# Performance work log

Measured on AMD Instinct MI355X. Metric: run time of the kernel, lower is better.

## Reference

```python
import jax, jax.numpy as jnp
import numpy as np
import math

H = 8
C = 512
HIDE = 2048
LN_EPS = 1e-6


def setup_inputs() -> dict:
    key = jax.random.key(0)
    ks = jax.random.split(key, 9)
    B, N = 4, 2048
    std = 0.02
    return {
        "q": jax.random.normal(ks[0], (B, N, C), jnp.float32),
        "k": jax.random.normal(ks[1], (B, N, C), jnp.float32),
        "v": jax.random.normal(ks[2], (B, N, C), jnp.float32),
        "fc1_w": jax.random.normal(ks[3], (HIDE, C), jnp.float32) * std,
        "fc1_b": jnp.zeros((HIDE,), jnp.float32),
        "fc2_w": jax.random.normal(ks[4], (C, HIDE), jnp.float32) * std,
        "fc2_b": jnp.zeros((C,), jnp.float32),
        "ln1_w": jnp.ones((C,), jnp.float32),
        "ln1_b": jnp.zeros((C,), jnp.float32),
        "ln2_w": jnp.ones((C,), jnp.float32),
        "ln2_b": jnp.zeros((C,), jnp.float32),
    }


def _layernorm(x, w, b):
    mu = jnp.mean(x, axis=-1, keepdims=True)
    var = jnp.var(x, axis=-1, keepdims=True)
    return (x - mu) * jax.lax.rsqrt(var + LN_EPS) * w + b


def _mha(q, k, v):
    B, N, _ = q.shape
    hd = C // H
    # [B, H, N, hd]
    qh = q.reshape(B, N, H, hd).transpose(0, 2, 1, 3)
    kh = k.reshape(B, N, H, hd).transpose(0, 2, 1, 3)
    vh = v.reshape(B, N, H, hd).transpose(0, 2, 1, 3)
    scores = jnp.einsum('bhqd,bhkd->bhqk', qh, kh) / math.sqrt(hd)
    probs = jax.nn.softmax(scores, axis=-1)
    out = jnp.einsum('bhqk,bhkd->bhqd', probs, vh)
    return out.transpose(0, 2, 1, 3).reshape(B, N, C)


def reference(q, k, v, fc1_w, fc1_b, fc2_w, fc2_b, ln1_w, ln1_b, ln2_w, ln2_b):
    attn = _mha(q, k, v)
    q2 = _layernorm(q + attn, ln1_w, ln1_b)
    h = jax.nn.gelu(q2 @ fc1_w.T + fc1_b, approximate=False)
    mlp = h @ fc2_w.T + fc2_b
    return _layernorm(q2 + mlp, ln2_w, ln2_b)
```

## Files before the change

kernel.cpp:

```cpp
#include <hip/hip_runtime.h>
#include <math.h>

typedef unsigned short u16;
typedef __bf16 bf16_t;
typedef bf16_t bf16x4 __attribute__((ext_vector_type(4)));
typedef bf16_t bf16x8 __attribute__((ext_vector_type(8)));
typedef short s16x4 __attribute__((ext_vector_type(4)));
typedef float f32x4 __attribute__((ext_vector_type(4)));

typedef const __attribute__((address_space(1))) void* gcp;
typedef __attribute__((address_space(3))) void* lcp;

#define BB 4
#define NN 2048
#define CC 512
#define HH 8
#define HD 64
#define HIDE_ 2048
#define TT (BB*NN)

#if __has_builtin(__builtin_amdgcn_exp2f)
#define EXP2(x) __builtin_amdgcn_exp2f(x)
#else
#define EXP2(x) __expf((x) * 0.69314718055994531f)
#endif

#if __has_builtin(__builtin_amdgcn_rcpf)
#define RCP(x) __builtin_amdgcn_rcpf(x)
#else
#define RCP(x) (1.0f / (x))
#endif

__device__ __forceinline__ u16 f2bf(float f) {
  unsigned u = __float_as_uint(f);
  u += 0x7FFF + ((u >> 16) & 1);
  return (u16)(u >> 16);
}

__device__ __forceinline__ int xcd_swz(int orig, int nwg) {
  return (orig & 7) * (nwg >> 3) + (orig >> 3);
}

__device__ __forceinline__ void bf8_to_f(const u16* p, float* f) {
  uint4 u = *(const uint4*)p;
  f[0] = __uint_as_float(u.x << 16); f[1] = __uint_as_float(u.x & 0xffff0000u);
  f[2] = __uint_as_float(u.y << 16); f[3] = __uint_as_float(u.y & 0xffff0000u);
  f[4] = __uint_as_float(u.z << 16); f[5] = __uint_as_float(u.z & 0xffff0000u);
  f[6] = __uint_as_float(u.w << 16); f[7] = __uint_as_float(u.w & 0xffff0000u);
}

__device__ __forceinline__ bf16x8 ldq8(const float* p, float s) {
  float4 a = *(const float4*)p;
  float4 b = *(const float4*)(p + 4);
  bf16x8 r = {(bf16_t)(a.x * s), (bf16_t)(a.y * s), (bf16_t)(a.z * s), (bf16_t)(a.w * s),
              (bf16_t)(b.x * s), (bf16_t)(b.y * s), (bf16_t)(b.z * s), (bf16_t)(b.w * s)};
  return r;
}

__device__ __forceinline__ float gelu_tanh(float x) {
  float y = 0.7978845608028654f * x * (1.0f + 0.044715f * x * x);
  float a = y * 2.8853900817779268f;
  a = fminf(fmaxf(a, -30.0f), 30.0f);
  float e = EXP2(a);
  float t = (e - 1.0f) * RCP(e + 1.0f);
  return 0.5f * x * (1.0f + t);
}

__global__ __launch_bounds__(256) void prep_kernel(const float* __restrict__ k,
                                                   const float* __restrict__ fc1w,
                                                   const float* __restrict__ fc2w,
                                                   const float* __restrict__ v,
                                                   u16* __restrict__ kb,
                                                   u16* __restrict__ w1b,
                                                   u16* __restrict__ w2b,
                                                   u16* __restrict__ vtb) {
  __shared__ __align__(16) u16 T[64 * 72];
  int bid = blockIdx.x, tid = threadIdx.x;
  if (bid < 3072) {
    const float* in;
    u16* out;
    int rel;
    if (bid < 2048)      { in = k;    out = kb;  rel = bid; }
    else if (bid < 2560) { in = fc1w; out = w1b; rel = bid - 2048; }
    else                 { in = fc2w; out = w2b; rel = bid - 2560; }
    int i = (rel * 256 + tid) * 8;
    float4 a = *(const float4*)(in + i);
    float4 b2 = *(const float4*)(in + i + 4);
    u16 r[8] = {f2bf(a.x), f2bf(a.y), f2bf(a.z), f2bf(a.w),
                f2bf(b2.x), f2bf(b2.y), f2bf(b2.z), f2bf(b2.w)};
    *(uint4*)(out + i) = *(const uint4*)r;
    return;
  }
  int tv = bid - 3072;
  int j0 = (tv & 31) * 64;
  int bh = tv >> 5;
  int b = bh >> 3, h = bh & 7;
#pragma unroll
  for (int i = 0; i < 16; i++) {
    int idx = i * 256 + tid;
    int j = idx >> 6, d = idx & 63;
    T[d * 72 + j] = f2bf(v[((size_t)(b * NN + j0 + j)) * CC + h * 64 + d]);
  }
  __syncthreads();
#pragma unroll
  for (int i = 0; i < 16; i++) {
    int idx = i * 256 + tid;
    int d = idx >> 6, j = idx & 63;
    vtb[((size_t)(bh * 64 + d)) * NN + j0 + j] = T[d * 72 + j];
  }
}

__global__ __launch_bounds__(256, 4) void attn_kernel(const float* __restrict__ qf,
                                                      const u16* __restrict__ kb,
                                                      const u16* __restrict__ vtb,
                                                      u16* __restrict__ ou,
                                                      float* __restrict__ lsum,
                                                      float qs) {
  __shared__ __align__(16) u16 Ks[64 * 64];
  __shared__ __align__(16) u16 Vs[64 * 64];
  int tid = threadIdx.x, wave = tid >> 6, lane = tid & 63;
  int l15 = lane & 15, quad = lane >> 4;
  int r7 = l15 & 7;
  int bid = xcd_swz(blockIdx.x, 512);
  int half = blockIdx.y;
  int qt = bid & 15, h = (bid >> 4) & 7, b = bid >> 7;
  int qw = qt * 128 + wave * 32;
  int j0base = half * 1024;

  u16* ou_ = ou + (size_t)half * TT * CC;
  float* ls_ = lsum + (size_t)half * TT * HH;

  const float* qp = qf + ((size_t)(b * NN + qw + l15)) * CC + h * 64 + quad * 8;
  bf16x8 qfA0 = ldq8(qp, qs);
  bf16x8 qfA1 = ldq8(qp + 32, qs);
  bf16x8 qfB0 = ldq8(qp + (size_t)16 * CC, qs);
  bf16x8 qfB1 = ldq8(qp + (size_t)16 * CC + 32, qs);

  int rl = lane >> 3;
  int cb = (lane & 7) ^ rl;
  int rK = wave * 16 + rl;
  size_t vtbase = ((size_t)(b * HH + h)) * 64 * NN;
  const u16* kp0 = kb + ((size_t)(b * NN + j0base + rK)) * CC + h * 64 + cb * 8;
  const u16* kp1 = kp0 + (size_t)8 * CC;
  const u16* vp0 = vtb + vtbase + (size_t)rK * NN + j0base + cb * 8;
  const u16* vp1 = vp0 + (size_t)8 * NN;
  lcp lK0 = (lcp)&Ks[wave * 16 * 64];
  lcp lK1 = (lcp)&Ks[wave * 16 * 64 + 8 * 64];
  lcp lV0 = (lcp)&Vs[wave * 16 * 64];
  lcp lV1 = (lcp)&Vs[wave * 16 * 64 + 8 * 64];

  float lA = 0.f, lB = 0.f;
  f32x4 oA[4] = {}, oB[4] = {};

  for (int kt = 0; kt < 16; kt++) {
    __syncthreads();
    __builtin_amdgcn_global_load_lds((gcp)kp0, lK0, 16, 0, 0);
    __builtin_amdgcn_global_load_lds((gcp)kp1, lK1, 16, 0, 0);
    __builtin_amdgcn_global_load_lds((gcp)vp0, lV0, 16, 0, 0);
    __builtin_amdgcn_global_load_lds((gcp)vp1, lV1, 16, 0, 0);
    kp0 += (size_t)64 * CC; kp1 += (size_t)64 * CC;
    vp0 += 64; vp1 += 64;
    __syncthreads();

    s16x4 pfA[4], pfB[4];
    __builtin_amdgcn_s_setprio(1);
#pragma unroll
    for (int nt = 0; nt < 4; nt++) {
      const u16* krow = &Ks[(nt * 16 + l15) * 64];
      bf16x8 k0 = *(const bf16x8*)&krow[(quad ^ r7) * 8];
      bf16x8 k1 = *(const bf16x8*)&krow[((quad + 4) ^ r7) * 8];
      f32x4 zA = {0.f, 0.f, 0.f, 0.f}, zB = {0.f, 0.f, 0.f, 0.f};
      zA = __builtin_amdgcn_mfma_f32_16x16x32_bf16(k0, qfA0, zA, 0, 0, 0);
      zA = __builtin_amdgcn_mfma_f32_16x16x32_bf16(k1, qfA1, zA, 0, 0, 0);
      zB = __builtin_amdgcn_mfma_f32_16x16x32_bf16(k0, qfB0, zB, 0, 0, 0);
      zB = __builtin_amdgcn_mfma_f32_16x16x32_bf16(k1, qfB1, zB, 0, 0, 0);
      float a0 = EXP2(zA[0]), a1 = EXP2(zA[1]), a2 = EXP2(zA[2]), a3 = EXP2(zA[3]);
      float b0 = EXP2(zB[0]), b1 = EXP2(zB[1]), b2 = EXP2(zB[2]), b3 = EXP2(zB[3]);
      lA += (a0 + a1) + (a2 + a3);
      lB += (b0 + b1) + (b2 + b3);
      bf16x4 ta = {(bf16_t)a0, (bf16_t)a1, (bf16_t)a2, (bf16_t)a3};
      bf16x4 tb = {(bf16_t)b0, (bf16_t)b1, (bf16_t)b2, (bf16_t)b3};
      pfA[nt] = __builtin_bit_cast(s16x4, ta);
      pfB[nt] = __builtin_bit_cast(s16x4, tb);
    }
#pragma unroll
    for (int dt = 0; dt < 4; dt++) {
      const u16* vrow = &Vs[(dt * 16 + l15) * 64];
#pragma unroll
      for (int nt = 0; nt < 4; nt++) {
        s16x4 vf = *(const s16x4*)
            &vrow[((nt * 2 + (quad >> 1)) ^ r7) * 8 + (quad & 1) * 4];
        oA[dt] = __builtin_amdgcn_mfma_f32_16x16x16bf16_1k(vf, pfA[nt], oA[dt], 0, 0, 0);
        oB[dt] = __builtin_amdgcn_mfma_f32_16x16x16bf16_1k(vf, pfB[nt], oB[dt], 0, 0, 0);
      }
    }
    __builtin_amdgcn_s_setprio(0);
  }

  lA += __shfl_xor(lA, 16, 64);
  lA += __shfl_xor(lA, 32, 64);
  lB += __shfl_xor(lB, 16, 64);
  lB += __shfl_xor(lB, 32, 64);
  if (quad == 0) {
    ls_[(size_t)(b * NN + qw + l15) * HH + h] = lA;
    ls_[(size_t)(b * NN + qw + 16 + l15) * HH + h] = lB;
  }
  size_t obase = ((size_t)(b * NN + qw + l15)) * CC + h * 64 + quad * 4;
#pragma unroll
  for (int dt = 0; dt < 4; dt++) {
    u16 ra[4] = {f2bf(oA[dt][0]), f2bf(oA[dt][1]), f2bf(oA[dt][2]), f2bf(oA[dt][3])};
    u16 rb[4] = {f2bf(oB[dt][0]), f2bf(oB[dt][1]), f2bf(oB[dt][2]), f2bf(oB[dt][3])};
    *(uint2*)&ou_[obase + dt * 16] = *(const uint2*)ra;
    *(uint2*)&ou_[obase + (size_t)16 * CC + dt * 16] = *(const uint2*)rb;
  }
}

__global__ __launch_bounds__(256) void ln1_kernel(const float* __restrict__ q,
                                                  const u16* __restrict__ ou,
                                                  const float* __restrict__ lsum,
                                                  const float* __restrict__ w,
                                                  const float* __restrict__ bb,
                                                  u16* __restrict__ outb) {
  int tid = threadIdx.x;
  int row = blockIdx.x * 4 + (tid >> 6);
  int lane = tid & 63;
  int h = lane >> 3;
  size_t base = (size_t)row * CC + lane * 8;
  const u16* ou1 = ou + (size_t)TT * CC;
  const float* ls1 = lsum + (size_t)TT * HH;
  float li = lsum[(size_t)row * HH + h] + ls1[(size_t)row * HH + h];
  float inv = 1.0f / li;
  float4 a0 = *(const float4*)(q + base);
  float4 a1 = *(const float4*)(q + base + 4);
  float c[8], d[8];
  bf8_to_f(ou + base, c);
  bf8_to_f(ou1 + base, d);
  float av[8] = {a0.x, a0.y, a0.z, a0.w, a1.x, a1.y, a1.z, a1.w};
  float x[8];
#pragma unroll
  for (int i = 0; i < 8; i++) x[i] = av[i] + (c[i] + d[i]) * inv;
  float sum = 0.f, sq = 0.f;
#pragma unroll
  for (int i = 0; i < 8; i++) { sum += x[i]; sq += x[i] * x[i]; }
#pragma unroll
  for (int msk = 1; msk < 64; msk <<= 1) {
    sum += __shfl_xor(sum, msk, 64);
    sq += __shfl_xor(sq, msk, 64);
  }
  float mu = sum * (1.0f / CC);
  float var = sq * (1.0f / CC) - mu * mu;
  float rs = rsqrtf(var + 1e-6f);
  int col = lane * 8;
  float4 w0 = *(const float4*)(w + col);
  float4 w1 = *(const float4*)(w + col + 4);
  float4 b0 = *(const float4*)(bb + col);
  float4 b1 = *(const float4*)(bb + col + 4);
  float wv[8] = {w0.x, w0.y, w0.z, w0.w, w1.x, w1.y, w1.z, w1.w};
  float bv[8] = {b0.x, b0.y, b0.z, b0.w, b1.x, b1.y, b1.z, b1.w};
  u16 r[8];
#pragma unroll
  for (int i = 0; i < 8; i++) r[i] = f2bf((x[i] - mu) * rs * wv[i] + bv[i]);
  *(uint4*)(outb + base) = *(const uint4*)r;
}

__global__ __launch_bounds__(256) void ln2_kernel(const u16* __restrict__ q2b,
                                                  const u16* __restrict__ mp,
                                                  const float* __restrict__ fb,
                                                  const float* __restrict__ w,
                                                  const float* __restrict__ bb,
                                                  float* __restrict__ outf) {
  int tid = threadIdx.x;
  int row = blockIdx.x * 4 + (tid >> 6);
  int lane = tid & 63;
  size_t base = (size_t)row * CC + lane * 8;
  const u16* mp1 = mp + (size_t)TT * CC;
  const u16* mp2 = mp + (size_t)2 * TT * CC;
  const u16* mp3 = mp + (size_t)3 * TT * CC;
  int col = lane * 8;
  float a[8], c[8], d[8], e[8], g[8];
  bf8_to_f(q2b + base, a);
  bf8_to_f(mp + base, c);
  bf8_to_f(mp1 + base, d);
  bf8_to_f(mp2 + base, e);
  bf8_to_f(mp3 + base, g);
  float4 f0 = *(const float4*)(fb + col);
  float4 f1 = *(const float4*)(fb + col + 4);
  float fbv[8] = {f0.x, f0.y, f0.z, f0.w, f1.x, f1.y, f1.z, f1.w};
  float x[8];
#pragma unroll
  for (int i = 0; i < 8; i++) x[i] = a[i] + ((c[i] + d[i]) + (e[i] + g[i])) + fbv[i];
  float sum = 0.f, sq = 0.f;
#pragma unroll
  for (int i = 0; i < 8; i++) { sum += x[i]; sq += x[i] * x[i]; }
#pragma unroll
  for (int msk = 1; msk < 64; msk <<= 1) {
    sum += __shfl_xor(sum, msk, 64);
    sq += __shfl_xor(sq, msk, 64);
  }
  float mu = sum * (1.0f / CC);
  float var = sq * (1.0f / CC) - mu * mu;
  float rs = rsqrtf(var + 1e-6f);
  float4 w0 = *(const float4*)(w + col);
  float4 w1 = *(const float4*)(w + col + 4);
  float4 b0 = *(const float4*)(bb + col);
  float4 b1 = *(const float4*)(bb + col + 4);
  float wv[8] = {w0.x, w0.y, w0.z, w0.w, w1.x, w1.y, w1.z, w1.w};
  float bv[8] = {b0.x, b0.y, b0.z, b0.w, b1.x, b1.y, b1.z, b1.w};
  float y[8];
#pragma unroll
  for (int i = 0; i < 8; i++) y[i] = (x[i] - mu) * rs * wv[i] + bv[i];
  *(float4*)(outf + base) = make_float4(y[0], y[1], y[2], y[3]);
  *(float4*)(outf + base + 4) = make_float4(y[4], y[5], y[6], y[7]);
}

#define GBAR() do { asm volatile("" ::: "memory"); __builtin_amdgcn_s_barrier(); \
                    asm volatile("" ::: "memory"); } while (0)

template <bool GELU>
__global__ __launch_bounds__(512, 2) void gemm256(const u16* __restrict__ A,
                                                  const u16* __restrict__ Bw,
                                                  const float* __restrict__ bias,
                                                  u16* __restrict__ outb,
                                                  int Nn, int K, int NT,
                                                  int gx, int gy) {
  __shared__ __align__(16) u16 As[2][256 * 64];
  __shared__ __align__(16) u16 Bs[2][256 * 64];
  int tid = threadIdx.x, wave = tid >> 6, lane = tid & 63;
  int l15 = lane & 15, quad = lane >> 4;
  int r7x = l15 & 7;
  int nwg = gridDim.x;
  int l = xcd_swz(blockIdx.x, nwg);
  int bx = l % gx;
  int by = (l / gx) % gy;
  int bz = l / (gx * gy);
  int m0 = by * 256, n0 = bx * 256;
  int kbeg = bz * (NT * 64);
  u16* outz = outb + (size_t)bz * ((size_t)TT * CC);
  int wm = (wave >> 2) * 128, wn = (wave & 3) * 64;
  int rl = lane >> 3;
  int cb = (lane & 7) ^ rl;
  const size_t rowK8 = (size_t)8 * K, rowK128 = (size_t)128 * K;
  const u16* Ap = &A[(size_t)(m0 + wave * 16 + rl) * K + kbeg + cb * 8];
  const u16* Bp = &Bw[(size_t)(n0 + wave * 16 + rl) * K + kbeg + cb * 8];
  unsigned sbase = wave * 16 * 64;

  f32x4 acc[8][4] = {};

  auto stageA = [&](int buf, int kofs) {
#pragma unroll
    for (int half = 0; half < 2; half++) {
      const u16* p = Ap + kofs + (size_t)half * rowK128;
      __builtin_amdgcn_global_load_lds((gcp)p, (lcp)&As[buf][half * 8192 + sbase], 16, 0, 0);
      __builtin_amdgcn_global_load_lds((gcp)(p + rowK8), (lcp)&As[buf][half * 8192 + sbase + 512], 16, 0, 0);
    }
  };
  auto stageB = [&](int buf, int kofs) {
#pragma unroll
    for (int half = 0; half < 2; half++) {
      const u16* p = Bp + kofs + (size_t)half * rowK128;
      __builtin_amdgcn_global_load_lds((gcp)p, (lcp)&Bs[buf][half * 8192 + sbase], 16, 0, 0);
      __builtin_amdgcn_global_load_lds((gcp)(p + rowK8), (lcp)&Bs[buf][half * 8192 + sbase + 512], 16, 0, 0);
    }
  };

  stageB(0, 0); stageA(0, 0);
  stageB(1, 64); stageA(1, 64);
  asm volatile("s_waitcnt vmcnt(8)" ::: "memory");
  __builtin_amdgcn_s_barrier();

#define RDA(buf, mfr, kh) \
  (*(const bf16x8*)&As[buf][(wm + (mfr) * 16 + l15) * 64 + (((kh) * 4 + quad) ^ r7x) * 8])
#define RDB(buf, nfr, kh) \
  (*(const bf16x8*)&Bs[buf][(wn + (nfr) * 16 + l15) * 64 + (((kh) * 4 + quad) ^ r7x) * 8])
#define QMFMA(AM0, BN0, AF, BF)                                              \
  _Pragma("unroll") for (int am = 0; am < 4; am++)                           \
  _Pragma("unroll") for (int bn = 0; bn < 2; bn++)                           \
  _Pragma("unroll") for (int kh = 0; kh < 2; kh++)                           \
    acc[(AM0) + am][(BN0) + bn] = __builtin_amdgcn_mfma_f32_16x16x32_bf16(   \
        AF[am][kh], BF[bn][kh], acc[(AM0) + am][(BN0) + bn], 0, 0, 0);

  for (int t = 0; t < NT; t++) {
    int buf = t & 1;
    int kof2 = (t + 2) * 64;
    bool pf = (t + 2) < NT;
    bf16x8 aF[4][2], bLo[2][2], bHi[2][2];
#pragma unroll
    for (int am = 0; am < 4; am++)
#pragma unroll
      for (int kh = 0; kh < 2; kh++) aF[am][kh] = RDA(buf, am, kh);
#pragma unroll
    for (int bn = 0; bn < 2; bn++)
#pragma unroll
      for (int kh = 0; kh < 2; kh++) bLo[bn][kh] = RDB(buf, bn, kh);
    __builtin_amdgcn_s_setprio(1);
    QMFMA(0, 0, aF, bLo)
    __builtin_amdgcn_s_setprio(0);
    GBAR();
#pragma unroll
    for (int bn = 0; bn < 2; bn++)
#pragma unroll
      for (int kh = 0; kh < 2; kh++) bHi[bn][kh] = RDB(buf, 2 + bn, kh);
    __builtin_amdgcn_s_setprio(1);
    QMFMA(0, 2, aF, bHi)
    __builtin_amdgcn_s_setprio(0);
    GBAR();
#pragma unroll
    for (int am = 0; am < 4; am++)
#pragma unroll
      for (int kh = 0; kh < 2; kh++) aF[am][kh] = RDA(buf, 4 + am, kh);
    if (pf) stageB(buf, kof2);
    __builtin_amdgcn_s_setprio(1);
    QMFMA(4, 2, aF, bHi)
    __builtin_amdgcn_s_setprio(0);
    GBAR();
    if (pf) stageA(buf, kof2);
    __builtin_amdgcn_s_setprio(1);
    QMFMA(4, 0, aF, bLo)
    __builtin_amdgcn_s_setprio(0);
    if (t + 1 < NT) {
      if (pf) asm volatile("s_waitcnt vmcnt(8)" ::: "memory");
      else    asm volatile("s_waitcnt vmcnt(0)" ::: "memory");
      __builtin_amdgcn_s_barrier();
      asm volatile("" ::: "memory");
    }
  }
#undef RDA
#undef RDB
#undef QMFMA

#pragma unroll
  for (int am = 0; am < 8; am++)
#pragma unroll
    for (int bn = 0; bn < 4; bn++) {
      int rowi = m0 + wm + am * 16 + quad * 4;
      int col = n0 + wn + bn * 16 + l15;
      float bcol = GELU ? bias[col] : 0.0f;
#pragma unroll
      for (int r = 0; r < 4; r++) {
        float val = acc[am][bn][r] + bcol;
        if (GELU) val = gelu_tanh(val);
        outz[(size_t)(rowi + r) * Nn + col] = f2bf(val);
      }
    }
}

extern "C" void kernel_launch(void* const* d_in, const int* in_sizes, int n_in,
                              void* d_out, int out_size, void* d_ws, size_t ws_size,
                              hipStream_t stream) {
  const float* q = (const float*)d_in[0];
  const float* k = (const float*)d_in[1];
  const float* v = (const float*)d_in[2];
  const float* fc1_w = (const float*)d_in[3];
  const float* fc1_b = (const float*)d_in[4];
  const float* fc2_w = (const float*)d_in[5];
  const float* fc2_b = (const float*)d_in[6];
  const float* ln1_w = (const float*)d_in[7];
  const float* ln1_b = (const float*)d_in[8];
  const float* ln2_w = (const float*)d_in[9];
  const float* ln2_b = (const float*)d_in[10];
  float* out = (float*)d_out;

  char* ws = (char*)d_ws;
  size_t off = 0;
  u16* kb = (u16*)(ws + off); off += (size_t)TT * CC * 2;
  u16* vtb = (u16*)(ws + off); off += (size_t)TT * CC * 2;
  u16* w1b = (u16*)(ws + off); off += (size_t)HIDE_ * CC * 2;
  u16* w2b = (u16*)(ws + off); off += (size_t)CC * HIDE_ * 2;
  u16* ou = (u16*)(ws + off); off += (size_t)2 * TT * CC * 2;
  float* lsum = (float*)(ws + off); off += (size_t)2 * TT * HH * 4;
  u16* q2b = (u16*)(ws + off); off += (size_t)TT * CC * 2;
  u16* hbuf = (u16*)(ws + off); off += (size_t)TT * HIDE_ * 2;
  u16* mp = (u16*)(ws + off); off += (size_t)4 * TT * CC * 2;

  const float QS = 0.18033688011112042f;
  prep_kernel<<<4096, 256, 0, stream>>>(k, fc1_w, fc2_w, v, kb, w1b, w2b, vtb);
  attn_kernel<<<dim3(512, 2), 256, 0, stream>>>(q, kb, vtb, ou, lsum, QS);
  ln1_kernel<<<2048, 256, 0, stream>>>(q, ou, lsum, ln1_w, ln1_b, q2b);
  gemm256<true><<<256, 512, 0, stream>>>(q2b, w1b, fc1_b, hbuf, HIDE_, CC, 8, 8, 32);
  gemm256<false><<<256, 512, 0, stream>>>(hbuf, w2b, fc2_b, mp, CC, HIDE_, 8, 2, 32);
  ln2_kernel<<<2048, 256, 0, stream>>>(q2b, mp, fc2_b, ln2_w, ln2_b, out);
}
```

Baseline: 224.0 us.

## Replace 256x256 GEMM tiles with 128x128 tiles and simpler pipeline

Both MLP GEMMs switch from a 512-thread 256x256 tile kernel to a 256-thread 128x128 tile kernel, launched as 1024 workgroups instead of 256. The interleaved four-phase LDS read/MFMA/barrier schedule becomes two MFMA halves separated by one barrier, after which the next stage is prefetched. Smaller tiles give more workgroups for the CUs and possibly more occupancy. The cost is lower arithmetic intensity per tile, so operands are reloaded from global memory more often.

```diff
diff --git a/kernel.cpp b/kernel.cpp
--- a/kernel.cpp
+++ b/kernel.cpp
@@ -313,109 +313,87 @@
   *(float4*)(outf + base + 4) = make_float4(y[4], y[5], y[6], y[7]);
 }
 
-#define GBAR() do { asm volatile("" ::: "memory"); __builtin_amdgcn_s_barrier(); \
-                    asm volatile("" ::: "memory"); } while (0)
-
 template <bool GELU>
-__global__ __launch_bounds__(512, 2) void gemm256(const u16* __restrict__ A,
-                                                  const u16* __restrict__ Bw,
-                                                  const float* __restrict__ bias,
-                                                  u16* __restrict__ outb,
-                                                  int Nn, int K, int NT,
-                                                  int gx, int gy) {
-  __shared__ __align__(16) u16 As[2][256 * 64];
-  __shared__ __align__(16) u16 Bs[2][256 * 64];
+__global__ __launch_bounds__(256) void gemm128(const u16* __restrict__ A,
+                                               const u16* __restrict__ Bw,
+                                               const float* __restrict__ bias,
+                                               u16* __restrict__ outb,
+                                               int Nn, int K, int NT,
+                                               int gx, int gy) {
+  __shared__ __align__(16) u16 As[2][128 * 64];
+  __shared__ __align__(16) u16 Bs[2][128 * 64];
   int tid = threadIdx.x, wave = tid >> 6, lane = tid & 63;
   int l15 = lane & 15, quad = lane >> 4;
-  int r7x = l15 & 7;
-  int nwg = gridDim.x;
-  int l = xcd_swz(blockIdx.x, nwg);
+  int r7 = l15 & 7;
+  int l = xcd_swz(blockIdx.x, gridDim.x);
   int bx = l % gx;
   int by = (l / gx) % gy;
   int bz = l / (gx * gy);
-  int m0 = by * 256, n0 = bx * 256;
+  int m0 = by * 128, n0 = bx * 128;
   int kbeg = bz * (NT * 64);
   u16* outz = outb + (size_t)bz * ((size_t)TT * CC);
-  int wm = (wave >> 2) * 128, wn = (wave & 3) * 64;
+  int wm = (wave >> 1) * 64, wn = (wave & 1) * 64;
+  int w32 = wave * 32;
   int rl = lane >> 3;
   int cb = (lane & 7) ^ rl;
-  const size_t rowK8 = (size_t)8 * K, rowK128 = (size_t)128 * K;
-  const u16* Ap = &A[(size_t)(m0 + wave * 16 + rl) * K + kbeg + cb * 8];
-  const u16* Bp = &Bw[(size_t)(n0 + wave * 16 + rl) * K + kbeg + cb * 8];
-  unsigned sbase = wave * 16 * 64;
-
-  f32x4 acc[8][4] = {};
-
-  auto stageA = [&](int buf, int kofs) {
-#pragma unroll
-    for (int half = 0; half < 2; half++) {
-      const u16* p = Ap + kofs + (size_t)half * rowK128;
-      __builtin_amdgcn_global_load_lds((gcp)p, (lcp)&As[buf][half * 8192 + sbase], 16, 0, 0);
-      __builtin_amdgcn_global_load_lds((gcp)(p + rowK8), (lcp)&As[buf][half * 8192 + sbase + 512], 16, 0, 0);
+  const u16* Ap = &A[(size_t)(m0 + w32 + rl) * K + kbeg + cb * 8];
+  const u16* Bp = &Bw[(size_t)(n0 + w32 + rl) * K + kbeg + cb * 8];
+  unsigned sb = w32 * 64;
+
+  f32x4 acc[4][4] = {};
+
+  auto stage = [&](int buf, int kofs) {
+#pragma unroll
+    for (int c = 0; c < 4; c++) {
+      __builtin_amdgcn_global_load_lds((gcp)(Ap + kofs + (size_t)(c * 8) * K),
+          (lcp)&As[buf][sb + c * 512], 16, 0, 0);
+      __builtin_amdgcn_global_load_lds((gcp)(Bp + kofs + (size_t)(c * 8) * K),
+          (lcp)&Bs[buf][sb + c * 512], 16, 0, 0);
     }
   };
-  auto stageB = [&](int buf, int kofs) {
-#pragma unroll
-    for (int half = 0; half < 2; half++) {
-      const u16* p = Bp + kofs + (size_t)half * rowK128;
-      __builtin_amdgcn_global_load_lds((gcp)p, (lcp)&Bs[buf][half * 8192 + sbase], 16, 0, 0);
-      __builtin_amdgcn_global_load_lds((gcp)(p + rowK8), (lcp)&Bs[buf][half * 8192 + sbase + 512], 16, 0, 0);
-    }
-  };
-
-  stageB(0, 0); stageA(0, 0);
-  stageB(1, 64); stageA(1, 64);
+
+  stage(0, 0);
+  stage(1, 64);
   asm volatile("s_waitcnt vmcnt(8)" ::: "memory");
   __builtin_amdgcn_s_barrier();
 
-#define RDA(buf, mfr, kh) \
-  (*(const bf16x8*)&As[buf][(wm + (mfr) * 16 + l15) * 64 + (((kh) * 4 + quad) ^ r7x) * 8])
-#define RDB(buf, nfr, kh) \
-  (*(const bf16x8*)&Bs[buf][(wn + (nfr) * 16 + l15) * 64 + (((kh) * 4 + quad) ^ r7x) * 8])
-#define QMFMA(AM0, BN0, AF, BF)                                              \
-  _Pragma("unroll") for (int am = 0; am < 4; am++)                           \
-  _Pragma("unroll") for (int bn = 0; bn < 2; bn++)                           \
-  _Pragma("unroll") for (int kh = 0; kh < 2; kh++)                           \
-    acc[(AM0) + am][(BN0) + bn] = __builtin_amdgcn_mfma_f32_16x16x32_bf16(   \
-        AF[am][kh], BF[bn][kh], acc[(AM0) + am][(BN0) + bn], 0, 0, 0);
-
   for (int t = 0; t < NT; t++) {
     int buf = t & 1;
-    int kof2 = (t + 2) * 64;
     bool pf = (t + 2) < NT;
-    bf16x8 aF[4][2], bLo[2][2], bHi[2][2];
-#pragma unroll
-    for (int am = 0; am < 4; am++)
-#pragma unroll
-      for (int kh = 0; kh < 2; kh++) aF[am][kh] = RDA(buf, am, kh);
-#pragma unroll
-    for (int bn = 0; bn < 2; bn++)
-#pragma unroll
-      for (int kh = 0; kh < 2; kh++) bLo[bn][kh] = RDB(buf, bn, kh);
+    bf16x8 aF[4][2], bF[4][2];
+#pragma unroll
+    for (int m = 0; m < 4; m++)
+#pragma unroll
+      for (int kh = 0; kh < 2; kh++)
+        aF[m][kh] = *(const bf16x8*)&As[buf][(wm + m * 16 + l15) * 64 +
+                                            ((kh * 4 + quad) ^ r7) * 8];
+#pragma unroll
+    for (int n = 0; n < 4; n++)
+#pragma unroll
+      for (int kh = 0; kh < 2; kh++)
+        bF[n][kh] = *(const bf16x8*)&Bs[buf][(wn + n * 16 + l15) * 64 +
+                                            ((kh * 4 + quad) ^ r7) * 8];
     __builtin_amdgcn_s_setprio(1);
-    QMFMA(0, 0, aF, bLo)
+#pragma unroll
+    for (int m = 0; m < 4; m++)
+#pragma unroll
+      for (int n = 0; n < 2; n++)
+#pragma unroll
+        for (int kh = 0; kh < 2; kh++)
+          acc[m][n] = __builtin_amdgcn_mfma_f32_16x16x32_bf16(aF[m][kh], bF[n][kh],
+                                                              acc[m][n], 0, 0, 0);
     __builtin_amdgcn_s_setprio(0);
-    GBAR();
-#pragma unroll
-    for (int bn = 0; bn < 2; bn++)
-#pragma unroll
-      for (int kh = 0; kh < 2; kh++) bHi[bn][kh] = RDB(buf, 2 + bn, kh);
+    asm volatile("s_waitcnt lgkmcnt(0)\n\ts_barrier" ::: "memory");
+    if (pf) stage(buf, (t + 2) * 64);
     __builtin_amdgcn_s_setprio(1);
-    QMFMA(0, 2, aF, bHi)
-    __builtin_amdgcn_s_setprio(0);
-    GBAR();
-#pragma unroll
-    for (int am = 0; am < 4; am++)
-#pragma unroll
-      for (int kh = 0; kh < 2; kh++) aF[am][kh] = RDA(buf, 4 + am, kh);
-    if (pf) stageB(buf, kof2);
-    __builtin_amdgcn_s_setprio(1);
-    QMFMA(4, 2, aF, bHi)
-    __builtin_amdgcn_s_setprio(0);
-    GBAR();
-    if (pf) stageA(buf, kof2);
-    __builtin_amdgcn_s_setprio(1);
-    QMFMA(4, 0, aF, bLo)
+#pragma unroll
+    for (int m = 0; m < 4; m++)
+#pragma unroll
+      for (int n = 2; n < 4; n++)
+#pragma unroll
+        for (int kh = 0; kh < 2; kh++)
+          acc[m][n] = __builtin_amdgcn_mfma_f32_16x16x32_bf16(aF[m][kh], bF[n][kh],
+                                                              acc[m][n], 0, 0, 0);
     __builtin_amdgcn_s_setprio(0);
     if (t + 1 < NT) {
       if (pf) asm volatile("s_waitcnt vmcnt(8)" ::: "memory");
@@ -424,12 +402,9 @@
       asm volatile("" ::: "memory");
     }
   }
-#undef RDA
-#undef RDB
-#undef QMFMA
-
-#pragma unroll
-  for (int am = 0; am < 8; am++)
+
+#pragma unroll
+  for (int am = 0; am < 4; am++)
 #pragma unroll
     for (int bn = 0; bn < 4; bn++) {
       int rowi = m0 + wm + am * 16 + quad * 4;
@@ -476,7 +451,7 @@
   prep_kernel<<<4096, 256, 0, stream>>>(k, fc1_w, fc2_w, v, kb, w1b, w2b, vtb);
   attn_kernel<<<dim3(512, 2), 256, 0, stream>>>(q, kb, vtb, ou, lsum, QS);
   ln1_kernel<<<2048, 256, 0, stream>>>(q, ou, lsum, ln1_w, ln1_b, q2b);
-  gemm256<true><<<256, 512, 0, stream>>>(q2b, w1b, fc1_b, hbuf, HIDE_, CC, 8, 8, 32);
-  gemm256<false><<<256, 512, 0, stream>>>(hbuf, w2b, fc2_b, mp, CC, HIDE_, 8, 2, 32);
+  gemm128<true><<<1024, 256, 0, stream>>>(q2b, w1b, fc1_b, hbuf, HIDE_, CC, 8, 16, 64);
+  gemm128<false><<<1024, 256, 0, stream>>>(hbuf, w2b, fc2_b, mp, CC, HIDE_, 8, 4, 64);
   ln2_kernel<<<2048, 256, 0, stream>>>(q2b, mp, fc2_b, ln2_w, ln2_b, out);
 }
```

Result: no change. 222.3 us (-0.7%).
